# Performance work log

Hardware: AMD Instinct MI355X
Metric: run time of the kernel (lower is better)

Reference implementation:

```python
import jax, jax.numpy as jnp
import numpy as np

IN, OUT, RANK, ALPHA, GS = 4096, 4096, 16, 32, 64
SCALING = ALPHA / RANK  # alpha / rank = 2.0


def setup_inputs() -> dict:
    key = jax.random.key(0)
    k1, k2, k3, k4, k5 = jax.random.split(key, 5)
    x = jax.random.normal(k1, (4, 2048, IN), dtype=jnp.float32)
    # signed int4 codes in [-8, 7]
    q_w = jax.random.randint(k2, (OUT, IN), -8, 8, dtype=jnp.int32)
    # per-group absmax scales (positive, small)
    scales = jax.random.uniform(k3, (OUT, IN // GS), dtype=jnp.float32) * 0.02 + 1e-3
    lora_A = jax.random.normal(k4, (RANK, IN), dtype=jnp.float32) * 0.02
    lora_B = jax.random.normal(k5, (OUT, RANK), dtype=jnp.float32) * 0.02
    return {"x": x, "q_w": q_w, "scales": scales, "lora_A": lora_A, "lora_B": lora_B}


def reference(x, q_w, scales, lora_A, lora_B):
    # Dequantize 4-bit base weight: blockwise symmetric, group_size=GS along in_features.
    # W[o, g*GS + j] = q[o, g*GS + j] * scales[o, g]
    W = (q_w.astype(jnp.float32).reshape(OUT, IN // GS, GS)
         * scales[:, :, None]).reshape(OUT, IN)
    # Frozen base layer: y = x @ W^T (Linear4bit, no bias)
    base_output = jnp.einsum('bsi,oi->bso', x, W)
    # LoRA branch (dropout p=0 -> identity): B(A(x)) * (alpha/rank)
    lora_output = jnp.einsum('bsr,or->bso', jnp.einsum('bsi,ri->bsr', x, lora_A), lora_B) * SCALING
    return base_output + lora_output
```

## Files before the change

### kernel.cpp

```cpp
#include <hip/hip_runtime.h>
#include <hip/hip_bf16.h>


typedef unsigned short u16;
typedef __attribute__((ext_vector_type(8))) short bf16x8;
typedef __attribute__((ext_vector_type(4))) float f32x4;

#define M_DIM 8192
#define N_DIM 4096
#define K_DIM 4096
#define BM 256
#define BN 256
#define BK 32
#define KT_MAIN 128
#define NT 129

__device__ static inline u16 f2bf(float f) {
    union { float f; unsigned u; } v; v.f = f;
    unsigned r = v.u + 0x7fffu + ((v.u >> 16) & 1u);
    return (u16)(r >> 16);
}

__device__ static inline void gload16(const void* g, void* s) {
    __builtin_amdgcn_global_load_lds(
        (const __attribute__((address_space(1))) void*)g,
        (__attribute__((address_space(3))) void*)s, 16, 0, 0);
}

__global__ __launch_bounds__(256) void wprep_kernel(
        const int* __restrict__ q, const float* __restrict__ scales,
        u16* __restrict__ Wb) {
    int idx = blockIdx.x * 256 + threadIdx.x;
    int o  = idx >> 9;
    int kc = (idx & 511) << 3;
    float s = scales[(o << 6) + (kc >> 6)];
    const int4* qp = (const int4*)(q + (size_t)o * K_DIM + kc);
    int4 q0 = qp[0], q1 = qp[1];
    ushort4 r0, r1;
    r0.x = f2bf((float)q0.x * s); r0.y = f2bf((float)q0.y * s);
    r0.z = f2bf((float)q0.z * s); r0.w = f2bf((float)q0.w * s);
    r1.x = f2bf((float)q1.x * s); r1.y = f2bf((float)q1.y * s);
    r1.z = f2bf((float)q1.z * s); r1.w = f2bf((float)q1.w * s);
    *(ushort4*)&Wb[(size_t)o * K_DIM + kc]     = r0;
    *(ushort4*)&Wb[(size_t)o * K_DIM + kc + 4] = r1;
}

__global__ __launch_bounds__(256) void bprep_kernel(
        const float* __restrict__ lora_B, u16* __restrict__ B2) {
    int idx = blockIdx.x * 256 + threadIdx.x;
    int o = idx >> 5, r = idx & 31;
    B2[idx] = (r < 16) ? f2bf(lora_B[o * 16 + r]) : (u16)0;
}

__global__ __launch_bounds__(256) void xprep_kernel(
        const float* __restrict__ x, const float* __restrict__ lora_A,
        u16* __restrict__ xb, u16* __restrict__ t2) {
    const int tid = threadIdx.x, w = tid >> 6, l = tid & 63;
    const int rb = blockIdx.x * 8 + w * 2;
    float acc[2][16];
#pragma unroll
    for (int j = 0; j < 2; ++j)
#pragma unroll
        for (int r = 0; r < 16; ++r) acc[j][r] = 0.f;

    for (int i = 0; i < 16; ++i) {
        int k0 = i * 256 + l * 4;
        float4 x0 = *(const float4*)&x[(size_t)rb * K_DIM + k0];
        float4 x1 = *(const float4*)&x[(size_t)(rb + 1) * K_DIM + k0];
        ushort4 o0, o1;
        o0.x = f2bf(x0.x); o0.y = f2bf(x0.y); o0.z = f2bf(x0.z); o0.w = f2bf(x0.w);
        o1.x = f2bf(x1.x); o1.y = f2bf(x1.y); o1.z = f2bf(x1.z); o1.w = f2bf(x1.w);
        *(ushort4*)&xb[(size_t)rb * K_DIM + k0]       = o0;
        *(ushort4*)&xb[(size_t)(rb + 1) * K_DIM + k0] = o1;
#pragma unroll
        for (int r = 0; r < 16; ++r) {
            float4 av = *(const float4*)&lora_A[(size_t)r * K_DIM + k0];
            acc[0][r] += x0.x * av.x + x0.y * av.y + x0.z * av.z + x0.w * av.w;
            acc[1][r] += x1.x * av.x + x1.y * av.y + x1.z * av.z + x1.w * av.w;
        }
    }
#pragma unroll
    for (int j = 0; j < 2; ++j)
#pragma unroll
        for (int r = 0; r < 16; ++r) {
            float v = acc[j][r];
            v += __shfl_xor(v, 32); v += __shfl_xor(v, 16);
            v += __shfl_xor(v, 8);  v += __shfl_xor(v, 4);
            v += __shfl_xor(v, 2);  v += __shfl_xor(v, 1);
            acc[j][r] = v;
        }
    float v = 0.f;
#pragma unroll
    for (int j = 0; j < 2; ++j)
#pragma unroll
        for (int r = 0; r < 16; ++r)
            if (l == j * 16 + r) v = acc[j][r];
    int row = (l >> 4) & 1, col = (l & 15) + ((l >= 32) ? 16 : 0);
    u16 outv = (l < 32) ? f2bf(2.0f * v) : (u16)0;
    t2[(size_t)(rb + row) * 32 + col] = outv;
}

__global__ __launch_bounds__(512, 2) void qlora_gemm(
        const u16* __restrict__ xb, const u16* __restrict__ Wb,
        const u16* __restrict__ t2, const u16* __restrict__ B2,
        float* __restrict__ out) {
    __shared__ u16 lds[3][16384];
    int bid = blockIdx.x;
    int swz = (bid & 7) * 64 + (bid >> 3);
    int bn = swz >> 5;
    int bm = swz & 31;
    const int tid = threadIdx.x, w = tid >> 6, l = tid & 63;
    const int wr = w >> 2, wc = w & 3;
    const int fr = l & 15, fq = l >> 4;
    const int sA = fq ^ ((fr >> 1) & 3);

    const int rs   = w * 16 + (l >> 2);
    const int sl16 = ((l & 3) ^ ((l >> 3) & 3)) << 4;
    const char* aRow0 = (const char*)xb + (((size_t)(bm * 256 + rs)) << 13) + sl16;
    const char* aRow1 = aRow0 + (size_t)(128u << 13);
    const char* bRow0 = (const char*)Wb + (((size_t)(bn * 256 + rs)) << 13) + sl16;
    const char* bRow1 = bRow0 + (size_t)(128u << 13);
    const char* aL0 = (const char*)t2 + (size_t)(bm * 256 + rs) * 64 + sl16;
    const char* aL1 = aL0 + 128 * 64;
    const char* bL0 = (const char*)B2 + (size_t)(bn * 256 + rs) * 64 + sl16;
    const char* bL1 = bL0 + 128 * 64;
    char* ldsC = (char*)&lds[0][0];
    const int dA = w * 1024;
    const int dB = 16384 + w * 1024;

    const int aoff = (wr * 128 + fr) * 64 + sA * 16;
    const int boff = 16384 + (wc * 64 + fr) * 64 + sA * 16;

    f32x4 acc[8][4] = {};

    auto stage = [&](int kt, int buf) {
        char* base = ldsC + buf * 32768;
        if (kt < KT_MAIN) {
            size_t ko = (size_t)kt * 64;
            gload16(aRow0 + ko, base + dA);
            gload16(aRow1 + ko, base + dA + 8192);
            gload16(bRow0 + ko, base + dB);
            gload16(bRow1 + ko, base + dB + 8192);
        } else {
            gload16(aL0, base + dA);
            gload16(aL1, base + dA + 8192);
            gload16(bL0, base + dB);
            gload16(bL1, base + dB + 8192);
        }
    };

    stage(0, 0);
    stage(1, 1);
    asm volatile("s_waitcnt vmcnt(4)" ::: "memory");
    __builtin_amdgcn_s_barrier();
    asm volatile("" ::: "memory");

    for (int t = 0; t < NT; ++t) {
        const int bufC = t % 3;
        if (t + 2 < NT) stage(t + 2, (t + 2) % 3);
        const char* cb = ldsC + bufC * 32768;
        bf16x8 af[8], bfr[4];
#pragma unroll
        for (int j = 0; j < 4; ++j)
            bfr[j] = *(const bf16x8*)(cb + boff + j * 1024);
#pragma unroll
        for (int i = 0; i < 8; ++i)
            af[i] = *(const bf16x8*)(cb + aoff + i * 1024);
        __builtin_amdgcn_s_setprio(1);
#pragma unroll
        for (int i = 0; i < 8; ++i)
#pragma unroll
            for (int j = 0; j < 4; ++j)
                acc[i][j] = __builtin_amdgcn_mfma_f32_16x16x32_bf16(
                                af[i], bfr[j], acc[i][j], 0, 0, 0);
        __builtin_amdgcn_s_setprio(0);
        if (t + 1 < NT) {
            if (t + 2 < NT)
                asm volatile("s_waitcnt vmcnt(4)" ::: "memory");
            else
                asm volatile("s_waitcnt vmcnt(0)" ::: "memory");
            __builtin_amdgcn_s_barrier();
            asm volatile("" ::: "memory");
        }
    }

    float* obase = out + (size_t)(bm * 256 + wr * 128 + fq * 4) * N_DIM
                       + bn * 256 + wc * 64 + fr;
#pragma unroll
    for (int i = 0; i < 8; ++i)
#pragma unroll
        for (int j = 0; j < 4; ++j)
#pragma unroll
            for (int r = 0; r < 4; ++r)
                obase[(size_t)(i * 16 + r) * N_DIM + j * 16] = acc[i][j][r];
}

extern "C" void kernel_launch(void* const* d_in, const int* in_sizes, int n_in,
                              void* d_out, int out_size, void* d_ws, size_t ws_size,
                              hipStream_t stream) {
    const float* x      = (const float*)d_in[0];
    const int*   qw     = (const int*)d_in[1];
    const float* scales = (const float*)d_in[2];
    const float* lora_A = (const float*)d_in[3];
    const float* lora_B = (const float*)d_in[4];
    float* out = (float*)d_out;

    char* ws = (char*)d_ws;
    u16* xb = (u16*)(ws);
    u16* Wb = (u16*)(ws + 67108864);
    u16* t2 = (u16*)(ws + 100663296);
    u16* B2 = (u16*)(ws + 101187584);

    wprep_kernel<<<8192, 256, 0, stream>>>(qw, scales, Wb);
    bprep_kernel<<<512, 256, 0, stream>>>(lora_B, B2);
    xprep_kernel<<<1024, 256, 0, stream>>>(x, lora_A, xb, t2);
    qlora_gemm<<<dim3(512), 512, 0, stream>>>(xb, Wb, t2, B2, out);
}
```

Before: 365.9 us.

## Split GEMM k-step into two phases interleaving A/B prefetch with MFMA halves

Each k-iteration of the main bf16 GEMM loop now runs in two halves. The first half loads four A fragments, then issues the A-tile prefetch and the first 16 MFMAs. The second half does the same with the B-tile prefetch and the remaining MFMAs. Extra workgroup barriers and sched_barriers fix the instruction order so global loads overlap compute in a ping-pong style. This adds two more barriers per iteration and lowers A-fragment register pressure, at the cost of more synchronisation overhead.

```diff
diff --git a/kernel.cpp b/kernel.cpp
--- a/kernel.cpp
+++ b/kernel.cpp
@@ -133,47 +133,79 @@
 
     f32x4 acc[8][4] = {};
 
-    auto stage = [&](int kt, int buf) {
+    auto stageA = [&](int kt, int buf) {
         char* base = ldsC + buf * 32768;
         if (kt < KT_MAIN) {
             size_t ko = (size_t)kt * 64;
             gload16(aRow0 + ko, base + dA);
             gload16(aRow1 + ko, base + dA + 8192);
+        } else {
+            gload16(aL0, base + dA);
+            gload16(aL1, base + dA + 8192);
+        }
+    };
+    auto stageB = [&](int kt, int buf) {
+        char* base = ldsC + buf * 32768;
+        if (kt < KT_MAIN) {
+            size_t ko = (size_t)kt * 64;
             gload16(bRow0 + ko, base + dB);
             gload16(bRow1 + ko, base + dB + 8192);
         } else {
-            gload16(aL0, base + dA);
-            gload16(aL1, base + dA + 8192);
             gload16(bL0, base + dB);
             gload16(bL1, base + dB + 8192);
         }
     };
 
-    stage(0, 0);
-    stage(1, 1);
+    stageA(0, 0); stageB(0, 0);
+    stageA(1, 1); stageB(1, 1);
     asm volatile("s_waitcnt vmcnt(4)" ::: "memory");
     __builtin_amdgcn_s_barrier();
     asm volatile("" ::: "memory");
 
     for (int t = 0; t < NT; ++t) {
-        const int bufC = t % 3;
-        if (t + 2 < NT) stage(t + 2, (t + 2) % 3);
-        const char* cb = ldsC + bufC * 32768;
-        bf16x8 af[8], bfr[4];
+        const char* cb = ldsC + (t % 3) * 32768;
+
+        bf16x8 bfr[4], af[4];
 #pragma unroll
         for (int j = 0; j < 4; ++j)
             bfr[j] = *(const bf16x8*)(cb + boff + j * 1024);
 #pragma unroll
-        for (int i = 0; i < 8; ++i)
+        for (int i = 0; i < 4; ++i)
             af[i] = *(const bf16x8*)(cb + aoff + i * 1024);
+        __builtin_amdgcn_sched_barrier(0);
+        if (t + 2 < NT) stageA(t + 2, (t + 2) % 3);
+        __builtin_amdgcn_s_barrier();
+        asm volatile("s_waitcnt lgkmcnt(0)" ::: "memory");
+        __builtin_amdgcn_sched_barrier(0);
         __builtin_amdgcn_s_setprio(1);
 #pragma unroll
-        for (int i = 0; i < 8; ++i)
+        for (int i = 0; i < 4; ++i)
 #pragma unroll
             for (int j = 0; j < 4; ++j)
                 acc[i][j] = __builtin_amdgcn_mfma_f32_16x16x32_bf16(
                                 af[i], bfr[j], acc[i][j], 0, 0, 0);
         __builtin_amdgcn_s_setprio(0);
+        __builtin_amdgcn_sched_barrier(0);
+        __builtin_amdgcn_s_barrier();
+
+        bf16x8 af2[4];
+#pragma unroll
+        for (int i = 0; i < 4; ++i)
+            af2[i] = *(const bf16x8*)(cb + aoff + (i + 4) * 1024);
+        __builtin_amdgcn_sched_barrier(0);
+        if (t + 2 < NT) stageB(t + 2, (t + 2) % 3);
+        __builtin_amdgcn_s_barrier();
+        asm volatile("s_waitcnt lgkmcnt(0)" ::: "memory");
+        __builtin_amdgcn_sched_barrier(0);
+        __builtin_amdgcn_s_setprio(1);
+#pragma unroll
+        for (int i = 0; i < 4; ++i)
+#pragma unroll
+            for (int j = 0; j < 4; ++j)
+                acc[i + 4][j] = __builtin_amdgcn_mfma_f32_16x16x32_bf16(
+                                    af2[i], bfr[j], acc[i + 4][j], 0, 0, 0);
+        __builtin_amdgcn_s_setprio(0);
+        __builtin_amdgcn_sched_barrier(0);
         if (t + 1 < NT) {
             if (t + 2 < NT)
                 asm volatile("s_waitcnt vmcnt(4)" ::: "memory");
```

Measured after the change: 379.3 us. 3.7% more time.

## Switch GEMM to BK=64 double-buffered pipeline with 8-way swizzle and nontemporal loads

Applied to the files above, without the earlier changes.

The GEMM K-tile grows from 32 to 64, halving the number of main-loop iterations and barriers. The LDS ring changes from a triple-buffered 32 KB-per-stage layout to a double-buffered 64 KB-per-stage layout with an 8-way XOR swizzle. The LoRA tail tile is padded to 64 columns, and the prep kernels are changed to match. The prep kernels also use nontemporal loads for the streamed x and q inputs. In exchange, each iteration now waits on its prefetch with vmcnt(0), so there is less load/compute overlap, and the doubled LDS (128 KB) may limit occupancy to one block per CU.

```diff
diff --git a/kernel.cpp b/kernel.cpp
--- a/kernel.cpp
+++ b/kernel.cpp
@@ -5,15 +5,14 @@
 typedef unsigned short u16;
 typedef __attribute__((ext_vector_type(8))) short bf16x8;
 typedef __attribute__((ext_vector_type(4))) float f32x4;
+typedef __attribute__((ext_vector_type(4))) int i32x4;
 
 #define M_DIM 8192
 #define N_DIM 4096
 #define K_DIM 4096
-#define BM 256
-#define BN 256
-#define BK 32
-#define KT_MAIN 128
-#define NT 129
+#define BK 64
+#define KT_MAIN 64
+#define NT 65
 
 __device__ static inline u16 f2bf(float f) {
     union { float f; unsigned u; } v; v.f = f;
@@ -34,8 +33,9 @@
     int o  = idx >> 9;
     int kc = (idx & 511) << 3;
     float s = scales[(o << 6) + (kc >> 6)];
-    const int4* qp = (const int4*)(q + (size_t)o * K_DIM + kc);
-    int4 q0 = qp[0], q1 = qp[1];
+    const i32x4* qp = (const i32x4*)(q + (size_t)o * K_DIM + kc);
+    i32x4 q0 = __builtin_nontemporal_load(qp);
+    i32x4 q1 = __builtin_nontemporal_load(qp + 1);
     ushort4 r0, r1;
     r0.x = f2bf((float)q0.x * s); r0.y = f2bf((float)q0.y * s);
     r0.z = f2bf((float)q0.z * s); r0.w = f2bf((float)q0.w * s);
@@ -48,7 +48,7 @@
 __global__ __launch_bounds__(256) void bprep_kernel(
         const float* __restrict__ lora_B, u16* __restrict__ B2) {
     int idx = blockIdx.x * 256 + threadIdx.x;
-    int o = idx >> 5, r = idx & 31;
+    int o = idx >> 6, r = idx & 63;
     B2[idx] = (r < 16) ? f2bf(lora_B[o * 16 + r]) : (u16)0;
 }
 
@@ -65,8 +65,10 @@
 
     for (int i = 0; i < 16; ++i) {
         int k0 = i * 256 + l * 4;
-        float4 x0 = *(const float4*)&x[(size_t)rb * K_DIM + k0];
-        float4 x1 = *(const float4*)&x[(size_t)(rb + 1) * K_DIM + k0];
+        f32x4 x0 = __builtin_nontemporal_load(
+                        (const f32x4*)&x[(size_t)rb * K_DIM + k0]);
+        f32x4 x1 = __builtin_nontemporal_load(
+                        (const f32x4*)&x[(size_t)(rb + 1) * K_DIM + k0]);
         ushort4 o0, o1;
         o0.x = f2bf(x0.x); o0.y = f2bf(x0.y); o0.z = f2bf(x0.z); o0.w = f2bf(x0.w);
         o1.x = f2bf(x1.x); o1.y = f2bf(x1.y); o1.z = f2bf(x1.z); o1.w = f2bf(x1.w);
@@ -74,7 +76,7 @@
         *(ushort4*)&xb[(size_t)(rb + 1) * K_DIM + k0] = o1;
 #pragma unroll
         for (int r = 0; r < 16; ++r) {
-            float4 av = *(const float4*)&lora_A[(size_t)r * K_DIM + k0];
+            f32x4 av = *(const f32x4*)&lora_A[(size_t)r * K_DIM + k0];
             acc[0][r] += x0.x * av.x + x0.y * av.y + x0.z * av.z + x0.w * av.w;
             acc[1][r] += x1.x * av.x + x1.y * av.y + x1.z * av.z + x1.w * av.w;
         }
@@ -89,22 +91,21 @@
             v += __shfl_xor(v, 2);  v += __shfl_xor(v, 1);
             acc[j][r] = v;
         }
-    float v = 0.f;
+    float lo = 0.f, hi = 0.f;
 #pragma unroll
     for (int j = 0; j < 2; ++j)
 #pragma unroll
-        for (int r = 0; r < 16; ++r)
-            if (l == j * 16 + r) v = acc[j][r];
-    int row = (l >> 4) & 1, col = (l & 15) + ((l >= 32) ? 16 : 0);
-    u16 outv = (l < 32) ? f2bf(2.0f * v) : (u16)0;
-    t2[(size_t)(rb + row) * 32 + col] = outv;
+        for (int c = 0; c < 8; ++c)
+            if (l == j * 32 + c) { lo = acc[j][2 * c]; hi = acc[j][2 * c + 1]; }
+    unsigned pack = (unsigned)f2bf(2.0f * lo) | ((unsigned)f2bf(2.0f * hi) << 16);
+    *(unsigned*)&t2[(size_t)(rb + (l >> 5)) * 64 + (l & 31) * 2] = pack;
 }
 
 __global__ __launch_bounds__(512, 2) void qlora_gemm(
         const u16* __restrict__ xb, const u16* __restrict__ Wb,
         const u16* __restrict__ t2, const u16* __restrict__ B2,
         float* __restrict__ out) {
-    __shared__ u16 lds[3][16384];
+    __shared__ u16 lds[2][32768];
     int bid = blockIdx.x;
     int swz = (bid & 7) * 64 + (bid >> 3);
     int bn = swz >> 5;
@@ -112,73 +113,89 @@
     const int tid = threadIdx.x, w = tid >> 6, l = tid & 63;
     const int wr = w >> 2, wc = w & 3;
     const int fr = l & 15, fq = l >> 4;
-    const int sA = fq ^ ((fr >> 1) & 3);
-
-    const int rs   = w * 16 + (l >> 2);
-    const int sl16 = ((l & 3) ^ ((l >> 3) & 3)) << 4;
-    const char* aRow0 = (const char*)xb + (((size_t)(bm * 256 + rs)) << 13) + sl16;
-    const char* aRow1 = aRow0 + (size_t)(128u << 13);
-    const char* bRow0 = (const char*)Wb + (((size_t)(bn * 256 + rs)) << 13) + sl16;
-    const char* bRow1 = bRow0 + (size_t)(128u << 13);
-    const char* aL0 = (const char*)t2 + (size_t)(bm * 256 + rs) * 64 + sl16;
-    const char* aL1 = aL0 + 128 * 64;
-    const char* bL0 = (const char*)B2 + (size_t)(bn * 256 + rs) * 64 + sl16;
-    const char* bL1 = bL0 + 128 * 64;
+    const int s0 = fq ^ (fr & 7);
+
+    const int sw16 = ((l & 7) ^ ((l >> 3) & 7)) << 4;
+    const int rl   = w * 8 + (l >> 3);
+    size_t offA[4], offB[4], lOffA[4], lOffB[4];
+#pragma unroll
+    for (int o = 0; o < 4; ++o) {
+        int rA = bm * 256 + o * 64 + rl;
+        int rB = bn * 256 + o * 64 + rl;
+        offA[o]  = (size_t)rA * 8192 + sw16;
+        offB[o]  = (size_t)rB * 8192 + sw16;
+        lOffA[o] = (size_t)rA * 128 + sw16;
+        lOffB[o] = (size_t)rB * 128 + sw16;
+    }
     char* ldsC = (char*)&lds[0][0];
-    const int dA = w * 1024;
-    const int dB = 16384 + w * 1024;
-
-    const int aoff = (wr * 128 + fr) * 64 + sA * 16;
-    const int boff = 16384 + (wc * 64 + fr) * 64 + sA * 16;
+    const int dst = w * 1024 + l * 16;
+
+    const int arow = (wr * 128 + fr) * 128;
+    const int brow = 32768 + (wc * 64 + fr) * 128;
 
     f32x4 acc[8][4] = {};
 
     auto stage = [&](int kt, int buf) {
-        char* base = ldsC + buf * 32768;
+        char* base = ldsC + buf * 65536;
         if (kt < KT_MAIN) {
-            size_t ko = (size_t)kt * 64;
-            gload16(aRow0 + ko, base + dA);
-            gload16(aRow1 + ko, base + dA + 8192);
-            gload16(bRow0 + ko, base + dB);
-            gload16(bRow1 + ko, base + dB + 8192);
+            size_t ko = (size_t)kt * 128;
+#pragma unroll
+            for (int o = 0; o < 4; ++o) {
+                gload16((const char*)xb + offA[o] + ko, base + dst + o * 8192);
+                gload16((const char*)Wb + offB[o] + ko, base + 32768 + dst + o * 8192);
+            }
         } else {
-            gload16(aL0, base + dA);
-            gload16(aL1, base + dA + 8192);
-            gload16(bL0, base + dB);
-            gload16(bL1, base + dB + 8192);
+#pragma unroll
+            for (int o = 0; o < 4; ++o) {
+                gload16((const char*)t2 + lOffA[o], base + dst + o * 8192);
+                gload16((const char*)B2 + lOffB[o], base + 32768 + dst + o * 8192);
+            }
         }
     };
 
     stage(0, 0);
-    stage(1, 1);
-    asm volatile("s_waitcnt vmcnt(4)" ::: "memory");
+    asm volatile("s_waitcnt vmcnt(0)" ::: "memory");
     __builtin_amdgcn_s_barrier();
     asm volatile("" ::: "memory");
 
     for (int t = 0; t < NT; ++t) {
-        const int bufC = t % 3;
-        if (t + 2 < NT) stage(t + 2, (t + 2) % 3);
-        const char* cb = ldsC + bufC * 32768;
-        bf16x8 af[8], bfr[4];
+        const char* cb = ldsC + (t & 1) * 65536;
+        if (t + 1 < NT) stage(t + 1, (t + 1) & 1);
+
+        bf16x8 a0[8], b0[4];
 #pragma unroll
         for (int j = 0; j < 4; ++j)
-            bfr[j] = *(const bf16x8*)(cb + boff + j * 1024);
-#pragma unroll
-        for (int i = 0; i < 8; ++i)
-            af[i] = *(const bf16x8*)(cb + aoff + i * 1024);
+            b0[j] = *(const bf16x8*)(cb + brow + j * 2048 + s0 * 16);
+#pragma unroll
+        for (int i = 0; i < 8; ++i)
+            a0[i] = *(const bf16x8*)(cb + arow + i * 2048 + s0 * 16);
         __builtin_amdgcn_s_setprio(1);
 #pragma unroll
         for (int i = 0; i < 8; ++i)
 #pragma unroll
             for (int j = 0; j < 4; ++j)
                 acc[i][j] = __builtin_amdgcn_mfma_f32_16x16x32_bf16(
-                                af[i], bfr[j], acc[i][j], 0, 0, 0);
+                                a0[i], b0[j], acc[i][j], 0, 0, 0);
         __builtin_amdgcn_s_setprio(0);
+
+        bf16x8 a1[8], b1[4];
+#pragma unroll
+        for (int j = 0; j < 4; ++j)
+            b1[j] = *(const bf16x8*)(cb + brow + j * 2048 + (s0 ^ 4) * 16);
+#pragma unroll
+        for (int i = 0; i < 8; ++i)
+            a1[i] = *(const bf16x8*)(cb + arow + i * 2048 + (s0 ^ 4) * 16);
+        __builtin_amdgcn_s_setprio(1);
+#pragma unroll
+        for (int i = 0; i < 8; ++i)
+#pragma unroll
+            for (int j = 0; j < 4; ++j)
+                acc[i][j] = __builtin_amdgcn_mfma_f32_16x16x32_bf16(
+                                a1[i], b1[j], acc[i][j], 0, 0, 0);
+        __builtin_amdgcn_s_setprio(0);
+
         if (t + 1 < NT) {
-            if (t + 2 < NT)
-                asm volatile("s_waitcnt vmcnt(4)" ::: "memory");
-            else
-                asm volatile("s_waitcnt vmcnt(0)" ::: "memory");
+            asm volatile("s_waitcnt vmcnt(0)" ::: "memory");
             __builtin_amdgcn_s_barrier();
             asm volatile("" ::: "memory");
         }
@@ -209,10 +226,10 @@
     u16* xb = (u16*)(ws);
     u16* Wb = (u16*)(ws + 67108864);
     u16* t2 = (u16*)(ws + 100663296);
-    u16* B2 = (u16*)(ws + 101187584);
+    u16* B2 = (u16*)(ws + 101711872);
 
     wprep_kernel<<<8192, 256, 0, stream>>>(qw, scales, Wb);
-    bprep_kernel<<<512, 256, 0, stream>>>(lora_B, B2);
+    bprep_kernel<<<1024, 256, 0, stream>>>(lora_B, B2);
     xprep_kernel<<<1024, 256, 0, stream>>>(x, lora_A, xb, t2);
     qlora_gemm<<<dim3(512), 512, 0, stream>>>(xb, Wb, t2, B2, out);
 }
```

After: 322.0 us. 12.0% less time.
